# Performance work log

Measured on AMD Instinct MI355X. Metric: run time of the kernel, lower is better.

## Reference

```python
import jax, jax.numpy as jnp
import numpy as np

N, E, D, H = 100000, 1600000, 128, 4
HD = D // H  # per-head dim


def setup_inputs() -> dict:
    key = jax.random.key(0)
    ks = jax.random.split(key, 16)
    s = 1.0 / np.sqrt(D)
    inp = {
        "x": jax.random.normal(ks[0], (N, D), jnp.float32),
        "edge_index": jax.random.randint(ks[1], (2, E), 0, N, jnp.int64),
        # GCNConv params
        "w_gcn": jax.random.normal(ks[2], (D, D), jnp.float32) * s,
        "b_gcn": jnp.zeros((D,), jnp.float32),
        # TransformerConv params (lin_query/key/value, lin_skip, lin_beta)
        "w_q": jax.random.normal(ks[3], (D, D), jnp.float32) * s,
        "b_q": jnp.zeros((D,), jnp.float32),
        "w_k": jax.random.normal(ks[4], (D, D), jnp.float32) * s,
        "b_k": jnp.zeros((D,), jnp.float32),
        "w_v": jax.random.normal(ks[5], (D, D), jnp.float32) * s,
        "b_v": jnp.zeros((D,), jnp.float32),
        "w_skip": jax.random.normal(ks[6], (D, D), jnp.float32) * s,
        "b_skip": jnp.zeros((D,), jnp.float32),
        "w_beta": jax.random.normal(ks[7], (3 * D, 1), jnp.float32) * s,
        # LayerNorms
        "ln1_g": jnp.ones((D,), jnp.float32),
        "ln1_b": jnp.zeros((D,), jnp.float32),
        "ln2_g": jnp.ones((D,), jnp.float32),
        "ln2_b": jnp.zeros((D,), jnp.float32),
        # FFN
        "w1": jax.random.normal(ks[8], (D, 2 * D), jnp.float32) * s,
        "b1": jnp.zeros((2 * D,), jnp.float32),
        "w2": jax.random.normal(ks[9], (2 * D, D), jnp.float32) * (1.0 / np.sqrt(2 * D)),
        "b2": jnp.zeros((D,), jnp.float32),
        "local_weight": jnp.ones((1,), jnp.float32),
        "global_weight": jnp.ones((1,), jnp.float32),
    }
    return inp


def _layer_norm(x, g, b, eps=1e-5):
    mu = jnp.mean(x, axis=-1, keepdims=True)
    var = jnp.var(x, axis=-1, keepdims=True)
    return (x - mu) * jax.lax.rsqrt(var + eps) * g + b


def _gps_forward(x, edge_index, w_gcn, b_gcn, w_q, b_q, w_k, b_k, w_v, b_v,
                 w_skip, b_skip, w_beta, ln1_g, ln1_b, ln2_g, ln2_b,
                 w1, b1, w2, b2, local_weight, global_weight):
    src, dst = edge_index[0], edge_index[1]  # messages flow src -> dst

    # ---- GCNConv (add_self_loops=False), sym norm ----
    deg = jax.ops.segment_sum(jnp.ones((E,), x.dtype), dst, num_segments=N)
    dinv = jnp.where(deg > 0, jax.lax.rsqrt(jnp.maximum(deg, 1.0)), 0.0)
    norm = dinv[src] * dinv[dst]  # [E]
    h = x @ w_gcn  # [N, D]
    local_out = jax.ops.segment_sum(h[src] * norm[:, None], dst, num_segments=N) + b_gcn

    # ---- TransformerConv (heads=H, concat=True, beta=True) ----
    q = (x @ w_q + b_q).reshape(N, H, HD)
    k = (x @ w_k + b_k).reshape(N, H, HD)
    v = (x @ w_v + b_v).reshape(N, H, HD)
    scores = jnp.sum(q[dst] * k[src], axis=-1) / np.sqrt(HD)  # [E, H]
    m = jax.ops.segment_max(scores, dst, num_segments=N)      # [N, H]
    m = jnp.where(jnp.isfinite(m), m, 0.0)
    e = jnp.exp(scores - m[dst])                              # [E, H]
    denom = jax.ops.segment_sum(e, dst, num_segments=N)       # [N, H]
    alpha = e / denom[dst]                                    # [E, H]
    agg = jax.ops.segment_sum(v[src] * alpha[:, :, None], dst, num_segments=N)
    out_attn = agg.reshape(N, D)
    x_r = x @ w_skip + b_skip
    beta = jax.nn.sigmoid(
        jnp.concatenate([out_attn, x_r, out_attn - x_r], axis=-1) @ w_beta)  # [N,1]
    global_out = beta * x_r + (1.0 - beta) * out_attn

    # ---- combine + LN + FFN + LN ----
    xc = local_weight * local_out + global_weight * global_out
    xn = _layer_norm(xc + xc, ln1_g, ln1_b)
    ff = jnp.maximum(xn @ w1 + b1, 0.0) @ w2 + b2
    return _layer_norm(ff + xn, ln2_g, ln2_b)


def reference(x, edge_index, w_gcn, b_gcn, w_q, b_q, w_k, b_k, w_v, b_v,
              w_skip, b_skip, w_beta, ln1_g, ln1_b, ln2_g, ln2_b,
              w1, b1, w2, b2, local_weight, global_weight):
    return _gps_forward(x, edge_index, w_gcn, b_gcn, w_q, b_q, w_k, b_k, w_v, b_v,
                        w_skip, b_skip, w_beta, ln1_g, ln1_b, ln2_g, ln2_b,
                        w1, b1, w2, b2, local_weight, global_weight)
```

## Files before the change

### kernel.cpp

```cpp
#include <hip/hip_runtime.h>

typedef unsigned int u32;
typedef unsigned short u16;
typedef __attribute__((ext_vector_type(8))) short bf16x8;
typedef __attribute__((ext_vector_type(4))) float f32x4;

__device__ __forceinline__ float bf2f(u16 u){ return __uint_as_float(((u32)u) << 16); }
__device__ __forceinline__ float bf2f_lo(u32 u){ return __uint_as_float(u << 16); }
__device__ __forceinline__ float bf2f_hi(u32 u){ return __uint_as_float(u & 0xffff0000u); }
__device__ __forceinline__ u16 f2bf(float f){
  u32 x = __float_as_uint(f);
  return (u16)((x + 0x7fffu + ((x >> 16) & 1u)) >> 16);
}

__global__ void k_prep_all(const float* wq, const float* bq, const float* wsk, const float* bsk,
                           const float* wk, const float* bk, const float* wv, const float* bv,
                           const float* wg, const float* w1, const float* w2,
                           u16* WcatT, float* bcat, u16* w1T, u16* w2T){
  int idx = blockIdx.x * 256 + threadIdx.x;
  if (idx < 640 * 128){
    int col = idx >> 7, k = idx & 127;
    int blk = col >> 7, c = col & 127;
    const float* w = (blk==0)?wq:(blk==1)?wsk:(blk==2)?wk:(blk==3)?wv:wg;
    WcatT[idx] = f2bf(w[k * 128 + c]);
    if (k == 0){
      const float* b = (blk==0)?bq:(blk==1)?bsk:(blk==2)?bk:(blk==3)?bv:nullptr;
      bcat[col] = b ? b[c] : 0.0f;
    }
  } else if (idx < 640*128 + 256*128){
    int j = idx - 640*128; int c = j >> 7, k = j & 127;
    w1T[j] = f2bf(w1[k * 256 + c]);
  } else if (idx < 640*128 + 256*128 + 128*256){
    int j = idx - (640*128 + 256*128); int c = j >> 8, k = j & 255;
    w2T[j] = f2bf(w2[k * 128 + c]);
  }
}

__global__ void k_cvt(const float* __restrict__ x, u16* __restrict__ xB, int n){
  int i = (blockIdx.x * 256 + threadIdx.x) * 4;
  if (i >= n) return;
  float4 v = *(const float4*)(x + i);
  ushort4 o; o.x = f2bf(v.x); o.y = f2bf(v.y); o.z = f2bf(v.z); o.w = f2bf(v.w);
  *(ushort4*)(xB + i) = o;
}

__global__ void k_hist(const int* __restrict__ ei, int E, int* __restrict__ deg){
  int e = blockIdx.x * 256 + threadIdx.x;
  if (e >= E) return;
  atomicAdd(&deg[ei[E + e]], 1);
}
__global__ void k_scan_a(const int* __restrict__ deg, int N, int* __restrict__ bsum){
  __shared__ int sh[256];
  int b = blockIdx.x, t = threadIdx.x;
  int base = b * 1024 + t * 4, s = 0;
  #pragma unroll
  for (int j = 0; j < 4; j++){ int i = base + j; if (i < N) s += deg[i]; }
  sh[t] = s; __syncthreads();
  for (int off = 128; off > 0; off >>= 1){ if (t < off) sh[t] += sh[t + off]; __syncthreads(); }
  if (t == 0) bsum[b] = sh[0];
}
__global__ void k_scan_b(const int* __restrict__ bsum, int NB, int* __restrict__ boff){
  __shared__ int sh[1024];
  int t = threadIdx.x;
  int self = (t < NB) ? bsum[t] : 0;
  sh[t] = self; __syncthreads();
  for (int off = 1; off < 1024; off <<= 1){
    int v = sh[t]; int add = (t >= off) ? sh[t - off] : 0;
    __syncthreads(); sh[t] = v + add; __syncthreads();
  }
  if (t < NB) boff[t] = sh[t] - self;
}
__global__ void k_scan_c(const int* __restrict__ deg, int N, int E,
                         const int* __restrict__ boff, int* __restrict__ rowptr){
  __shared__ int sh[256];
  int b = blockIdx.x, t = threadIdx.x;
  int base = b * 1024 + t * 4;
  int d[4]; int ts = 0;
  #pragma unroll
  for (int j = 0; j < 4; j++){ int i = base + j; d[j] = (i < N) ? deg[i] : 0; ts += d[j]; }
  sh[t] = ts; __syncthreads();
  for (int off = 1; off < 256; off <<= 1){
    int v = sh[t]; int add = (t >= off) ? sh[t - off] : 0;
    __syncthreads(); sh[t] = v + add; __syncthreads();
  }
  int excl = sh[t] - ts + boff[b];
  #pragma unroll
  for (int j = 0; j < 4; j++){ int i = base + j; if (i < N) rowptr[i] = excl; excl += d[j]; }
  if (b == 0 && t == 0) rowptr[N] = E;
}
__global__ void k_dinv(const int* __restrict__ deg, int N, float* __restrict__ dinv){
  int i = blockIdx.x * 256 + threadIdx.x;
  if (i < N) dinv[i] = deg[i] > 0 ? rsqrtf((float)deg[i]) : 0.0f;
}
__global__ void k_csr(const int* __restrict__ ei, int E,
                      const int* __restrict__ rowptr, int* __restrict__ fill, int* __restrict__ csr){
  int e = blockIdx.x * 256 + threadIdx.x;
  if (e >= E) return;
  int d = ei[E + e];
  int pos = rowptr[d] + atomicAdd(&fill[d], 1);
  csr[pos] = ei[e];
}

__device__ __forceinline__ void stageTile(const u16* __restrict__ g, int ldg, int row0, int rclamp,
                                          int kofs, u16* lds){
  int t = threadIdx.x;
  #pragma unroll
  for (int p = 0; p < 8; p++){
    int chunk = p * 256 + t;
    int r = chunk >> 4;
    int cs = (chunk & 15) << 3;
    int rg = row0 + r; if (rg >= rclamp) rg = rclamp - 1;
    bf16x8 v = *(const bf16x8*)(g + (size_t)rg * ldg + kofs + cs);
    *(bf16x8*)(lds + r * 128 + (cs ^ ((r & 7) << 3))) = v;
  }
}
__device__ __forceinline__ bf16x8 ldFrag(const u16* lds, int r, int k0){
  return *(const bf16x8*)(lds + r * 128 + (k0 ^ ((r & 7) << 3)));
}

__global__ __launch_bounds__(256) void k_gemm1(const u16* __restrict__ xB, const u16* __restrict__ WcatT,
    const float* __restrict__ bcat, u16* __restrict__ qB, u16* __restrict__ xrB,
    u16* __restrict__ kvhB, int N){
  __shared__ u16 As[128 * 128];
  __shared__ u16 Bs[128 * 128];
  int row0 = blockIdx.x * 128, cb = blockIdx.y;
  stageTile(xB, 128, row0, N, 0, As);
  stageTile(WcatT, 128, cb * 128, 1 << 30, 0, Bs);
  __syncthreads();
  int t = threadIdx.x, l = t & 63, w = t >> 6;
  int wm = w >> 1, wn = w & 1;
  int c16 = l & 15, g = l >> 4;
  f32x4 acc[4][4];
  #pragma unroll
  for (int mi = 0; mi < 4; mi++)
    #pragma unroll
    for (int ni = 0; ni < 4; ni++) acc[mi][ni] = (f32x4){0.f, 0.f, 0.f, 0.f};
  #pragma unroll
  for (int kk = 0; kk < 4; kk++){
    int k0 = kk * 32 + g * 8;
    bf16x8 af[4], bfr[4];
    #pragma unroll
    for (int mi = 0; mi < 4; mi++) af[mi] = ldFrag(As, wm * 64 + mi * 16 + c16, k0);
    #pragma unroll
    for (int ni = 0; ni < 4; ni++) bfr[ni] = ldFrag(Bs, wn * 64 + ni * 16 + c16, k0);
    #pragma unroll
    for (int mi = 0; mi < 4; mi++)
      #pragma unroll
      for (int ni = 0; ni < 4; ni++)
        acc[mi][ni] = __builtin_amdgcn_mfma_f32_16x16x32_bf16(af[mi], bfr[ni], acc[mi][ni], 0, 0, 0);
  }
  u16* dst; int ld, cofs;
  if (cb == 0){ dst = qB;  ld = 128; cofs = 0; }
  else if (cb == 1){ dst = xrB; ld = 128; cofs = 0; }
  else { dst = kvhB; ld = 384; cofs = (cb - 2) * 128; }
  float bias[4];
  #pragma unroll
  for (int ni = 0; ni < 4; ni++) bias[ni] = bcat[cb * 128 + wn * 64 + ni * 16 + c16];
  #pragma unroll
  for (int mi = 0; mi < 4; mi++){
    #pragma unroll
    for (int r = 0; r < 4; r++){
      int row = row0 + wm * 64 + mi * 16 + g * 4 + r;
      if (row < N){
        #pragma unroll
        for (int ni = 0; ni < 4; ni++)
          dst[(size_t)row * ld + cofs + wn * 64 + ni * 16 + c16] = f2bf(acc[mi][ni][r] + bias[ni]);
      }
    }
  }
}

__global__ __launch_bounds__(256) void k_edge(const u16* __restrict__ qB, const u16* __restrict__ xrB,
    const u16* __restrict__ kvhB,
    const int* __restrict__ csr, const int* __restrict__ rowptr, const float* __restrict__ dinv,
    const float* __restrict__ bgcn, const float* __restrict__ wbeta,
    const float* __restrict__ lng, const float* __restrict__ lnb,
    const float* __restrict__ lwp, const float* __restrict__ gwp,
    float* __restrict__ xn, u16* __restrict__ xnB, int N){
  int lane = threadIdx.x & 63;
  int half = lane >> 5;
  int li = lane & 31;
  int d0 = li * 4;
  int n = blockIdx.x * 4 + (threadIdx.x >> 6);
  if (n >= N) return;
  int ro = rowptr[n], re = rowptr[n + 1];
  uint2 qu = *(const uint2*)(qB + (size_t)n * 128 + d0);
  float q0 = bf2f_lo(qu.x), q1 = bf2f_hi(qu.x), q2 = bf2f_lo(qu.y), q3 = bf2f_hi(qu.y);
  float av0 = 0, av1 = 0, av2 = 0, av3 = 0;
  float ah0 = 0, ah1 = 0, ah2 = 0, ah3 = 0;
  float den = 0;
  const float SC = 0.17677669529663687f;
  for (int e = ro + half; e < re; e += 2){
    int s = csr[e];
    const u16* fb = kvhB + (size_t)s * 384;
    uint2 ku = *(const uint2*)(fb + d0);
    uint2 vu = *(const uint2*)(fb + 128 + d0);
    uint2 hu = *(const uint2*)(fb + 256 + d0);
    float dv = dinv[s];
    float part = q0 * bf2f_lo(ku.x) + q1 * bf2f_hi(ku.x)
               + q2 * bf2f_lo(ku.y) + q3 * bf2f_hi(ku.y);
    part += __shfl_xor(part, 1);
    part += __shfl_xor(part, 2);
    part += __shfl_xor(part, 4);
    float p = __expf(part * SC);
    av0 += p * bf2f_lo(vu.x); av1 += p * bf2f_hi(vu.x);
    av2 += p * bf2f_lo(vu.y); av3 += p * bf2f_hi(vu.y);
    ah0 += dv * bf2f_lo(hu.x); ah1 += dv * bf2f_hi(hu.x);
    ah2 += dv * bf2f_lo(hu.y); ah3 += dv * bf2f_hi(hu.y);
    den += p;
  }
  den += __shfl_xor(den, 32);
  av0 += __shfl_xor(av0, 32); av1 += __shfl_xor(av1, 32);
  av2 += __shfl_xor(av2, 32); av3 += __shfl_xor(av3, 32);
  ah0 += __shfl_xor(ah0, 32); ah1 += __shfl_xor(ah1, 32);
  ah2 += __shfl_xor(ah2, 32); ah3 += __shfl_xor(ah3, 32);
  float inv_den = den > 0 ? 1.0f / den : 0.0f;
  float at0 = av0 * inv_den, at1 = av1 * inv_den, at2 = av2 * inv_den, at3 = av3 * inv_den;
  uint2 xru = *(const uint2*)(xrB + (size_t)n * 128 + d0);
  float xr0 = bf2f_lo(xru.x), xr1 = bf2f_hi(xru.x), xr2 = bf2f_lo(xru.y), xr3 = bf2f_hi(xru.y);
  float4 wb0 = *(const float4*)(wbeta + d0);
  float4 wb1 = *(const float4*)(wbeta + 128 + d0);
  float4 wb2 = *(const float4*)(wbeta + 256 + d0);
  float z = at0 * wb0.x + at1 * wb0.y + at2 * wb0.z + at3 * wb0.w
          + xr0 * wb1.x + xr1 * wb1.y + xr2 * wb1.z + xr3 * wb1.w
          + (at0 - xr0) * wb2.x + (at1 - xr1) * wb2.y
          + (at2 - xr2) * wb2.z + (at3 - xr3) * wb2.w;
  z += __shfl_xor(z, 1); z += __shfl_xor(z, 2); z += __shfl_xor(z, 4);
  z += __shfl_xor(z, 8); z += __shfl_xor(z, 16);
  float beta = 1.0f / (1.0f + __expf(-z));
  float dn = dinv[n];
  float4 bg = *(const float4*)(bgcn + d0);
  float l0 = dn * ah0 + bg.x, l1 = dn * ah1 + bg.y, l2 = dn * ah2 + bg.z, l3 = dn * ah3 + bg.w;
  float lw = lwp[0], gw = gwp[0];
  float ib = 1.0f - beta;
  float t0 = 2.0f * (lw * l0 + gw * (beta * xr0 + ib * at0));
  float t1 = 2.0f * (lw * l1 + gw * (beta * xr1 + ib * at1));
  float t2 = 2.0f * (lw * l2 + gw * (beta * xr2 + ib * at2));
  float t3 = 2.0f * (lw * l3 + gw * (beta * xr3 + ib * at3));
  float s = t0 + t1 + t2 + t3;
  float sq = t0*t0 + t1*t1 + t2*t2 + t3*t3;
  s += __shfl_xor(s, 1);  sq += __shfl_xor(sq, 1);
  s += __shfl_xor(s, 2);  sq += __shfl_xor(sq, 2);
  s += __shfl_xor(s, 4);  sq += __shfl_xor(sq, 4);
  s += __shfl_xor(s, 8);  sq += __shfl_xor(sq, 8);
  s += __shfl_xor(s, 16); sq += __shfl_xor(sq, 16);
  float mu = s * (1.0f / 128.0f);
  float var = sq * (1.0f / 128.0f) - mu * mu;
  float inv = rsqrtf(var + 1e-5f);
  if (half == 0){
    float4 gm = *(const float4*)(lng + d0);
    float4 bt = *(const float4*)(lnb + d0);
    float o0 = (t0 - mu) * inv * gm.x + bt.x;
    float o1 = (t1 - mu) * inv * gm.y + bt.y;
    float o2 = (t2 - mu) * inv * gm.z + bt.z;
    float o3 = (t3 - mu) * inv * gm.w + bt.w;
    *(float4*)(xn + (size_t)n * 128 + d0) = make_float4(o0, o1, o2, o3);
    uint2 pk;
    pk.x = (u32)f2bf(o0) | ((u32)f2bf(o1) << 16);
    pk.y = (u32)f2bf(o2) | ((u32)f2bf(o3) << 16);
    *(uint2*)(xnB + (size_t)n * 128 + d0) = pk;
  }
}

__global__ __launch_bounds__(256) void k_ffn1(const u16* __restrict__ xnB, const u16* __restrict__ w1T,
    const float* __restrict__ b1, u16* __restrict__ hid, int N){
  __shared__ u16 As[128 * 128];
  __shared__ u16 Bs[128 * 128];
  int row0 = blockIdx.x * 128, cb = blockIdx.y;
  stageTile(xnB, 128, row0, N, 0, As);
  stageTile(w1T, 128, cb * 128, 1 << 30, 0, Bs);
  __syncthreads();
  int t = threadIdx.x, l = t & 63, w = t >> 6;
  int wm = w >> 1, wn = w & 1;
  int c16 = l & 15, g = l >> 4;
  f32x4 acc[4][4];
  #pragma unroll
  for (int mi = 0; mi < 4; mi++)
    #pragma unroll
    for (int ni = 0; ni < 4; ni++) acc[mi][ni] = (f32x4){0.f, 0.f, 0.f, 0.f};
  #pragma unroll
  for (int kk = 0; kk < 4; kk++){
    int k0 = kk * 32 + g * 8;
    bf16x8 af[4], bfr[4];
    #pragma unroll
    for (int mi = 0; mi < 4; mi++) af[mi] = ldFrag(As, wm * 64 + mi * 16 + c16, k0);
    #pragma unroll
    for (int ni = 0; ni < 4; ni++) bfr[ni] = ldFrag(Bs, wn * 64 + ni * 16 + c16, k0);
    #pragma unroll
    for (int mi = 0; mi < 4; mi++)
      #pragma unroll
      for (int ni = 0; ni < 4; ni++)
        acc[mi][ni] = __builtin_amdgcn_mfma_f32_16x16x32_bf16(af[mi], bfr[ni], acc[mi][ni], 0, 0, 0);
  }
  float bias[4];
  #pragma unroll
  for (int ni = 0; ni < 4; ni++) bias[ni] = b1[cb * 128 + wn * 64 + ni * 16 + c16];
  #pragma unroll
  for (int mi = 0; mi < 4; mi++){
    #pragma unroll
    for (int r = 0; r < 4; r++){
      int row = row0 + wm * 64 + mi * 16 + g * 4 + r;
      if (row < N){
        #pragma unroll
        for (int ni = 0; ni < 4; ni++)
          hid[(size_t)row * 256 + cb * 128 + wn * 64 + ni * 16 + c16] =
              f2bf(fmaxf(acc[mi][ni][r] + bias[ni], 0.0f));
      }
    }
  }
}

__global__ __launch_bounds__(256) void k_ffn2(const u16* __restrict__ hid, const u16* __restrict__ w2T,
    const float* __restrict__ b2, const float* __restrict__ xnf,
    const float* __restrict__ g2, const float* __restrict__ bt2,
    float* __restrict__ out, int N){
  __shared__ u16 As[128 * 128];
  __shared__ u16 Bs[128 * 128];
  int row0 = blockIdx.x * 128;
  int t = threadIdx.x, l = t & 63, w = t >> 6;
  int c16 = l & 15, g = l >> 4;
  f32x4 acc[2][8];
  #pragma unroll
  for (int mi = 0; mi < 2; mi++)
    #pragma unroll
    for (int ni = 0; ni < 8; ni++) acc[mi][ni] = (f32x4){0.f, 0.f, 0.f, 0.f};
  for (int kc = 0; kc < 2; kc++){
    if (kc) __syncthreads();
    stageTile(hid, 256, row0, N, kc * 128, As);
    stageTile(w2T, 256, 0, 1 << 30, kc * 128, Bs);
    __syncthreads();
    #pragma unroll
    for (int kk = 0; kk < 4; kk++){
      int k0 = kk * 32 + g * 8;
      bf16x8 af[2], bfr[8];
      #pragma unroll
      for (int mi = 0; mi < 2; mi++) af[mi] = ldFrag(As, w * 32 + mi * 16 + c16, k0);
      #pragma unroll
      for (int ni = 0; ni < 8; ni++) bfr[ni] = ldFrag(Bs, ni * 16 + c16, k0);
      #pragma unroll
      for (int mi = 0; mi < 2; mi++)
        #pragma unroll
        for (int ni = 0; ni < 8; ni++)
          acc[mi][ni] = __builtin_amdgcn_mfma_f32_16x16x32_bf16(af[mi], bfr[ni], acc[mi][ni], 0, 0, 0);
    }
  }
  float b2c[8], g2c[8], btc[8];
  #pragma unroll
  for (int ni = 0; ni < 8; ni++){
    int col = ni * 16 + c16;
    b2c[ni] = b2[col]; g2c[ni] = g2[col]; btc[ni] = bt2[col];
  }
  #pragma unroll
  for (int mi = 0; mi < 2; mi++){
    #pragma unroll
    for (int r = 0; r < 4; r++){
      int row = row0 + w * 32 + mi * 16 + g * 4 + r;
      int rc = row < N ? row : N - 1;
      float z[8]; float s = 0.f, sq = 0.f;
      #pragma unroll
      for (int ni = 0; ni < 8; ni++){
        z[ni] = acc[mi][ni][r] + b2c[ni] + xnf[(size_t)rc * 128 + ni * 16 + c16];
        s += z[ni]; sq += z[ni] * z[ni];
      }
      s += __shfl_xor(s, 1); sq += __shfl_xor(sq, 1);
      s += __shfl_xor(s, 2); sq += __shfl_xor(sq, 2);
      s += __shfl_xor(s, 4); sq += __shfl_xor(sq, 4);
      s += __shfl_xor(s, 8); sq += __shfl_xor(sq, 8);
      float mu = s * (1.0f / 128.0f);
      float var = sq * (1.0f / 128.0f) - mu * mu;
      float inv = rsqrtf(var + 1e-5f);
      if (row < N){
        #pragma unroll
        for (int ni = 0; ni < 8; ni++)
          out[(size_t)row * 128 + ni * 16 + c16] = (z[ni] - mu) * inv * g2c[ni] + btc[ni];
      }
    }
  }
}

extern "C" void kernel_launch(void* const* d_in, const int* in_sizes, int n_in,
                              void* d_out, int out_size, void* d_ws, size_t ws_size,
                              hipStream_t stream){
  const float* x      = (const float*)d_in[0];
  const int*   ei     = (const int*)d_in[1];
  const float* w_gcn  = (const float*)d_in[2];
  const float* b_gcn  = (const float*)d_in[3];
  const float* w_q    = (const float*)d_in[4];
  const float* b_q    = (const float*)d_in[5];
  const float* w_k    = (const float*)d_in[6];
  const float* b_k    = (const float*)d_in[7];
  const float* w_v    = (const float*)d_in[8];
  const float* b_v    = (const float*)d_in[9];
  const float* w_skip = (const float*)d_in[10];
  const float* b_skip = (const float*)d_in[11];
  const float* w_beta = (const float*)d_in[12];
  const float* ln1_g  = (const float*)d_in[13];
  const float* ln1_b  = (const float*)d_in[14];
  const float* ln2_g  = (const float*)d_in[15];
  const float* ln2_b  = (const float*)d_in[16];
  const float* w1     = (const float*)d_in[17];
  const float* b1     = (const float*)d_in[18];
  const float* w2     = (const float*)d_in[19];
  const float* b2     = (const float*)d_in[20];
  const float* lw     = (const float*)d_in[21];
  const float* gw     = (const float*)d_in[22];
  int N = in_sizes[0] / 128;
  int E = in_sizes[1] / 2;
  float* outf = (float*)d_out;
  float* xn   = (float*)d_out;

  char* ws = (char*)d_ws;
  size_t off = 0;
  auto alloc = [&](size_t bytes) -> char* {
    char* p = ws + off; off += (bytes + 255) & ~(size_t)255; return p;
  };
  u16* kvhB   = (u16*)alloc((size_t)N * 384 * 2);
  u16* xrB    = (u16*)alloc((size_t)N * 128 * 2);
  u16* qB     = (u16*)alloc((size_t)N * 128 * 2);
  u16* xB     = (u16*)alloc((size_t)N * 128 * 2);
  int* csr    = (int*)alloc((size_t)E * 4);
  int* deg    = (int*)alloc((size_t)N * 4);
  int* rowptr = (int*)alloc((size_t)(N + 1) * 4);
  int* fill   = (int*)alloc((size_t)N * 4);
  float* dinv = (float*)alloc((size_t)N * 4);
  int NB = (N + 1023) >> 10;
  int* bsum   = (int*)alloc((size_t)NB * 4);
  int* boff   = (int*)alloc((size_t)NB * 4);
  u16* WcatT  = (u16*)alloc((size_t)640 * 128 * 2);
  float* bcat = (float*)alloc((size_t)640 * 4);
  u16* w1T    = (u16*)alloc((size_t)256 * 128 * 2);
  u16* w2T    = (u16*)alloc((size_t)128 * 256 * 2);
  u16* hid    = kvhB;
  u16* xnB    = xB;

  if (off > ws_size) return;

  hipMemsetAsync(deg, 0, (size_t)N * 4, stream);
  hipMemsetAsync(fill, 0, (size_t)N * 4, stream);

  k_prep_all<<<576, 256, 0, stream>>>(w_q, b_q, w_skip, b_skip, w_k, b_k, w_v, b_v, w_gcn,
                                      w1, w2, WcatT, bcat, w1T, w2T);
  k_cvt<<<(N * 128 / 4 + 255) / 256, 256, 0, stream>>>(x, xB, N * 128);
  k_hist<<<(E + 255) / 256, 256, 0, stream>>>(ei, E, deg);
  k_scan_a<<<NB, 256, 0, stream>>>(deg, N, bsum);
  k_scan_b<<<1, 1024, 0, stream>>>(bsum, NB, boff);
  k_scan_c<<<NB, 256, 0, stream>>>(deg, N, E, boff, rowptr);
  k_dinv<<<(N + 255) / 256, 256, 0, stream>>>(deg, N, dinv);
  k_csr<<<(E + 255) / 256, 256, 0, stream>>>(ei, E, rowptr, fill, csr);

  int MB = (N + 127) / 128;
  dim3 g1(MB, 5);
  k_gemm1<<<g1, 256, 0, stream>>>(xB, WcatT, bcat, qB, xrB, kvhB, N);
  k_edge<<<(N + 3) / 4, 256, 0, stream>>>(qB, xrB, kvhB, csr, rowptr, dinv, b_gcn, w_beta,
                                          ln1_g, ln1_b, lw, gw, xn, xnB, N);
  dim3 f1(MB, 2);
  k_ffn1<<<f1, 256, 0, stream>>>(xnB, w1T, b1, hid, N);
  k_ffn2<<<MB, 256, 0, stream>>>(hid, w2T, b2, xn, ln2_g, ln2_b, outf, N);
}
```

Measured before the change: 472.7 us.

## Fuse x conversion into gemm1, merge dinv into scan, drop fp32 xn buffer

Removes the separate fp32-to-bf16 conversion kernel by converting x while staging it into LDS inside gemm1. gemm1 now loops over all five weight column blocks per row tile, so each x tile is read once instead of five times, at the cost of 782 blocks instead of 3910 and serialised column blocks. dinv is computed in the scan kernel, which removes one launch. The fp32 xn intermediate write is dropped and ffn2 reads the bf16 copy for the residual, which lowers precision slightly.

```diff
diff --git a/kernel.cpp b/kernel.cpp
--- a/kernel.cpp
+++ b/kernel.cpp
@@ -36,14 +36,6 @@
   }
 }
 
-__global__ void k_cvt(const float* __restrict__ x, u16* __restrict__ xB, int n){
-  int i = (blockIdx.x * 256 + threadIdx.x) * 4;
-  if (i >= n) return;
-  float4 v = *(const float4*)(x + i);
-  ushort4 o; o.x = f2bf(v.x); o.y = f2bf(v.y); o.z = f2bf(v.z); o.w = f2bf(v.w);
-  *(ushort4*)(xB + i) = o;
-}
-
 __global__ void k_hist(const int* __restrict__ ei, int E, int* __restrict__ deg){
   int e = blockIdx.x * 256 + threadIdx.x;
   if (e >= E) return;
@@ -71,7 +63,8 @@
   if (t < NB) boff[t] = sh[t] - self;
 }
 __global__ void k_scan_c(const int* __restrict__ deg, int N, int E,
-                         const int* __restrict__ boff, int* __restrict__ rowptr){
+                         const int* __restrict__ boff, int* __restrict__ rowptr,
+                         float* __restrict__ dinv){
   __shared__ int sh[256];
   int b = blockIdx.x, t = threadIdx.x;
   int base = b * 1024 + t * 4;
@@ -85,12 +78,15 @@
   }
   int excl = sh[t] - ts + boff[b];
   #pragma unroll
-  for (int j = 0; j < 4; j++){ int i = base + j; if (i < N) rowptr[i] = excl; excl += d[j]; }
+  for (int j = 0; j < 4; j++){
+    int i = base + j;
+    if (i < N){
+      rowptr[i] = excl;
+      dinv[i] = d[j] > 0 ? rsqrtf((float)d[j]) : 0.0f;
+    }
+    excl += d[j];
+  }
   if (b == 0 && t == 0) rowptr[N] = E;
-}
-__global__ void k_dinv(const int* __restrict__ deg, int N, float* __restrict__ dinv){
-  int i = blockIdx.x * 256 + threadIdx.x;
-  if (i < N) dinv[i] = deg[i] > 0 ? rsqrtf((float)deg[i]) : 0.0f;
 }
 __global__ void k_csr(const int* __restrict__ ei, int E,
                       const int* __restrict__ rowptr, int* __restrict__ fill, int* __restrict__ csr){
@@ -114,59 +110,81 @@
     *(bf16x8*)(lds + r * 128 + (cs ^ ((r & 7) << 3))) = v;
   }
 }
+__device__ __forceinline__ void stageTileF32(const float* __restrict__ g, int ldg, int row0,
+                                             int rclamp, u16* lds){
+  int t = threadIdx.x;
+  #pragma unroll
+  for (int p = 0; p < 8; p++){
+    int chunk = p * 256 + t;
+    int r = chunk >> 4;
+    int cs = (chunk & 15) << 3;
+    int rg = row0 + r; if (rg >= rclamp) rg = rclamp - 1;
+    const float* src = g + (size_t)rg * ldg + cs;
+    float4 a = *(const float4*)(src);
+    float4 b = *(const float4*)(src + 4);
+    u16* dst = lds + r * 128 + (cs ^ ((r & 7) << 3));
+    ushort4 lo; lo.x = f2bf(a.x); lo.y = f2bf(a.y); lo.z = f2bf(a.z); lo.w = f2bf(a.w);
+    ushort4 hi; hi.x = f2bf(b.x); hi.y = f2bf(b.y); hi.z = f2bf(b.z); hi.w = f2bf(b.w);
+    *(ushort4*)dst = lo;
+    *(ushort4*)(dst + 4) = hi;
+  }
+}
 __device__ __forceinline__ bf16x8 ldFrag(const u16* lds, int r, int k0){
   return *(const bf16x8*)(lds + r * 128 + (k0 ^ ((r & 7) << 3)));
 }
 
-__global__ __launch_bounds__(256) void k_gemm1(const u16* __restrict__ xB, const u16* __restrict__ WcatT,
+__global__ __launch_bounds__(256) void k_gemm1(const float* __restrict__ x, const u16* __restrict__ WcatT,
     const float* __restrict__ bcat, u16* __restrict__ qB, u16* __restrict__ xrB,
     u16* __restrict__ kvhB, int N){
   __shared__ u16 As[128 * 128];
   __shared__ u16 Bs[128 * 128];
-  int row0 = blockIdx.x * 128, cb = blockIdx.y;
-  stageTile(xB, 128, row0, N, 0, As);
-  stageTile(WcatT, 128, cb * 128, 1 << 30, 0, Bs);
-  __syncthreads();
+  int row0 = blockIdx.x * 128;
+  stageTileF32(x, 128, row0, N, As);
   int t = threadIdx.x, l = t & 63, w = t >> 6;
   int wm = w >> 1, wn = w & 1;
   int c16 = l & 15, g = l >> 4;
-  f32x4 acc[4][4];
-  #pragma unroll
-  for (int mi = 0; mi < 4; mi++)
-    #pragma unroll
-    for (int ni = 0; ni < 4; ni++) acc[mi][ni] = (f32x4){0.f, 0.f, 0.f, 0.f};
-  #pragma unroll
-  for (int kk = 0; kk < 4; kk++){
-    int k0 = kk * 32 + g * 8;
-    bf16x8 af[4], bfr[4];
-    #pragma unroll
-    for (int mi = 0; mi < 4; mi++) af[mi] = ldFrag(As, wm * 64 + mi * 16 + c16, k0);
-    #pragma unroll
-    for (int ni = 0; ni < 4; ni++) bfr[ni] = ldFrag(Bs, wn * 64 + ni * 16 + c16, k0);
+  for (int cb = 0; cb < 5; cb++){
+    stageTile(WcatT, 128, cb * 128, 1 << 30, 0, Bs);
+    __syncthreads();
+    f32x4 acc[4][4];
     #pragma unroll
     for (int mi = 0; mi < 4; mi++)
       #pragma unroll
-      for (int ni = 0; ni < 4; ni++)
-        acc[mi][ni] = __builtin_amdgcn_mfma_f32_16x16x32_bf16(af[mi], bfr[ni], acc[mi][ni], 0, 0, 0);
-  }
-  u16* dst; int ld, cofs;
-  if (cb == 0){ dst = qB;  ld = 128; cofs = 0; }
-  else if (cb == 1){ dst = xrB; ld = 128; cofs = 0; }
-  else { dst = kvhB; ld = 384; cofs = (cb - 2) * 128; }
-  float bias[4];
-  #pragma unroll
-  for (int ni = 0; ni < 4; ni++) bias[ni] = bcat[cb * 128 + wn * 64 + ni * 16 + c16];
-  #pragma unroll
-  for (int mi = 0; mi < 4; mi++){
-    #pragma unroll
-    for (int r = 0; r < 4; r++){
-      int row = row0 + wm * 64 + mi * 16 + g * 4 + r;
-      if (row < N){
+      for (int ni = 0; ni < 4; ni++) acc[mi][ni] = (f32x4){0.f, 0.f, 0.f, 0.f};
+    #pragma unroll
+    for (int kk = 0; kk < 4; kk++){
+      int k0 = kk * 32 + g * 8;
+      bf16x8 af[4], bfr[4];
+      #pragma unroll
+      for (int mi = 0; mi < 4; mi++) af[mi] = ldFrag(As, wm * 64 + mi * 16 + c16, k0);
+      #pragma unroll
+      for (int ni = 0; ni < 4; ni++) bfr[ni] = ldFrag(Bs, wn * 64 + ni * 16 + c16, k0);
+      #pragma unroll
+      for (int mi = 0; mi < 4; mi++)
         #pragma unroll
         for (int ni = 0; ni < 4; ni++)
-          dst[(size_t)row * ld + cofs + wn * 64 + ni * 16 + c16] = f2bf(acc[mi][ni][r] + bias[ni]);
+          acc[mi][ni] = __builtin_amdgcn_mfma_f32_16x16x32_bf16(af[mi], bfr[ni], acc[mi][ni], 0, 0, 0);
+    }
+    u16* dst; int ld, cofs;
+    if (cb == 0){ dst = qB;  ld = 128; cofs = 0; }
+    else if (cb == 1){ dst = xrB; ld = 128; cofs = 0; }
+    else { dst = kvhB; ld = 384; cofs = (cb - 2) * 128; }
+    float bias[4];
+    #pragma unroll
+    for (int ni = 0; ni < 4; ni++) bias[ni] = bcat[cb * 128 + wn * 64 + ni * 16 + c16];
+    #pragma unroll
+    for (int mi = 0; mi < 4; mi++){
+      #pragma unroll
+      for (int r = 0; r < 4; r++){
+        int row = row0 + wm * 64 + mi * 16 + g * 4 + r;
+        if (row < N){
+          #pragma unroll
+          for (int ni = 0; ni < 4; ni++)
+            dst[(size_t)row * ld + cofs + wn * 64 + ni * 16 + c16] = f2bf(acc[mi][ni][r] + bias[ni]);
+        }
       }
     }
+    __syncthreads();
   }
 }
 
@@ -176,7 +194,7 @@
     const float* __restrict__ bgcn, const float* __restrict__ wbeta,
     const float* __restrict__ lng, const float* __restrict__ lnb,
     const float* __restrict__ lwp, const float* __restrict__ gwp,
-    float* __restrict__ xn, u16* __restrict__ xnB, int N){
+    u16* __restrict__ xnB, int N){
   int lane = threadIdx.x & 63;
   int half = lane >> 5;
   int li = lane & 31;
@@ -254,7 +272,6 @@
     float o1 = (t1 - mu) * inv * gm.y + bt.y;
     float o2 = (t2 - mu) * inv * gm.z + bt.z;
     float o3 = (t3 - mu) * inv * gm.w + bt.w;
-    *(float4*)(xn + (size_t)n * 128 + d0) = make_float4(o0, o1, o2, o3);
     uint2 pk;
     pk.x = (u32)f2bf(o0) | ((u32)f2bf(o1) << 16);
     pk.y = (u32)f2bf(o2) | ((u32)f2bf(o3) << 16);
@@ -311,7 +328,7 @@
 }
 
 __global__ __launch_bounds__(256) void k_ffn2(const u16* __restrict__ hid, const u16* __restrict__ w2T,
-    const float* __restrict__ b2, const float* __restrict__ xnf,
+    const float* __restrict__ b2, const u16* __restrict__ xnB,
     const float* __restrict__ g2, const float* __restrict__ bt2,
     float* __restrict__ out, int N){
   __shared__ u16 As[128 * 128];
@@ -359,7 +376,8 @@
       float z[8]; float s = 0.f, sq = 0.f;
       #pragma unroll
       for (int ni = 0; ni < 8; ni++){
-        z[ni] = acc[mi][ni][r] + b2c[ni] + xnf[(size_t)rc * 128 + ni * 16 + c16];
+        float xv = bf2f(xnB[(size_t)rc * 128 + ni * 16 + c16]);
+        z[ni] = acc[mi][ni][r] + b2c[ni] + xv;
         s += z[ni]; sq += z[ni] * z[ni];
       }
       s += __shfl_xor(s, 1); sq += __shfl_xor(sq, 1);
@@ -407,7 +425,6 @@
   int N = in_sizes[0] / 128;
   int E = in_sizes[1] / 2;
   float* outf = (float*)d_out;
-  float* xn   = (float*)d_out;
 
   char* ws = (char*)d_ws;
   size_t off = 0;
@@ -417,7 +434,7 @@
   u16* kvhB   = (u16*)alloc((size_t)N * 384 * 2);
   u16* xrB    = (u16*)alloc((size_t)N * 128 * 2);
   u16* qB     = (u16*)alloc((size_t)N * 128 * 2);
-  u16* xB     = (u16*)alloc((size_t)N * 128 * 2);
+  u16* xnB    = (u16*)alloc((size_t)N * 128 * 2);
   int* csr    = (int*)alloc((size_t)E * 4);
   int* deg    = (int*)alloc((size_t)N * 4);
   int* rowptr = (int*)alloc((size_t)(N + 1) * 4);
@@ -431,7 +448,6 @@
   u16* w1T    = (u16*)alloc((size_t)256 * 128 * 2);
   u16* w2T    = (u16*)alloc((size_t)128 * 256 * 2);
   u16* hid    = kvhB;
-  u16* xnB    = xB;
 
   if (off > ws_size) return;
 
@@ -440,20 +456,17 @@
 
   k_prep_all<<<576, 256, 0, stream>>>(w_q, b_q, w_skip, b_skip, w_k, b_k, w_v, b_v, w_gcn,
                                       w1, w2, WcatT, bcat, w1T, w2T);
-  k_cvt<<<(N * 128 / 4 + 255) / 256, 256, 0, stream>>>(x, xB, N * 128);
   k_hist<<<(E + 255) / 256, 256, 0, stream>>>(ei, E, deg);
   k_scan_a<<<NB, 256, 0, stream>>>(deg, N, bsum);
   k_scan_b<<<1, 1024, 0, stream>>>(bsum, NB, boff);
-  k_scan_c<<<NB, 256, 0, stream>>>(deg, N, E, boff, rowptr);
-  k_dinv<<<(N + 255) / 256, 256, 0, stream>>>(deg, N, dinv);
+  k_scan_c<<<NB, 256, 0, stream>>>(deg, N, E, boff, rowptr, dinv);
   k_csr<<<(E + 255) / 256, 256, 0, stream>>>(ei, E, rowptr, fill, csr);
 
   int MB = (N + 127) / 128;
-  dim3 g1(MB, 5);
-  k_gemm1<<<g1, 256, 0, stream>>>(xB, WcatT, bcat, qB, xrB, kvhB, N);
+  k_gemm1<<<MB, 256, 0, stream>>>(x, WcatT, bcat, qB, xrB, kvhB, N);
   k_edge<<<(N + 3) / 4, 256, 0, stream>>>(qB, xrB, kvhB, csr, rowptr, dinv, b_gcn, w_beta,
-                                          ln1_g, ln1_b, lw, gw, xn, xnB, N);
+                                          ln1_g, ln1_b, lw, gw, xnB, N);
   dim3 f1(MB, 2);
   k_ffn1<<<f1, 256, 0, stream>>>(xnB, w1T, b1, hid, N);
-  k_ffn2<<<MB, 256, 0, stream>>>(hid, w2T, b2, xn, ln2_g, ln2_b, outf, N);
-}
+  k_ffn2<<<MB, 256, 0, stream>>>(hid, w2T, b2, xnB, ln2_g, ln2_b, outf, N);
+}
```

Measured after the change: 455.3 us. -3.7%, faster.
